# Performance work log

Hardware: AMD Instinct MI355X
Metric: run time of the kernel (lower is better)

## Reference

```python
import jax, jax.numpy as jnp
import numpy as np

NUM_NODES = 1_000_000
IN_FEATS = 128
NUM_GRAPHS = 1024
N_ITERS = 3


def setup_inputs() -> dict:
    key = jax.random.key(0)
    k1, k2, k3, k4, k5, k6 = jax.random.split(key, 6)
    H = IN_FEATS
    s = 1.0 / np.sqrt(H)
    x = jax.random.normal(k1, (NUM_NODES, H), dtype=jnp.float32)
    batch = jnp.sort(jax.random.randint(k2, (NUM_NODES,), 0, NUM_GRAPHS, dtype=jnp.int32))
    W_ih = jax.random.uniform(k3, (4 * H, 2 * H), minval=-s, maxval=s, dtype=jnp.float32)
    W_hh = jax.random.uniform(k4, (4 * H, H), minval=-s, maxval=s, dtype=jnp.float32)
    b_ih = jax.random.uniform(k5, (4 * H,), minval=-s, maxval=s, dtype=jnp.float32)
    b_hh = jax.random.uniform(k6, (4 * H,), minval=-s, maxval=s, dtype=jnp.float32)
    return {"x": x, "batch": batch, "W_ih": W_ih, "W_hh": W_hh, "b_ih": b_ih, "b_hh": b_hh}


def _lstm_cell(inp, h, c, W_ih, W_hh, b_ih, b_hh):
    # PyTorch gate order: i, f, g, o
    gates = inp @ W_ih.T + h @ W_hh.T + b_ih + b_hh  # (B, 4H)
    i, f, g, o = jnp.split(gates, 4, axis=-1)
    c_new = jax.nn.sigmoid(f) * c + jax.nn.sigmoid(i) * jnp.tanh(g)
    h_new = jax.nn.sigmoid(o) * jnp.tanh(c_new)
    return h_new, c_new


def reference(x, batch, W_ih, W_hh, b_ih, b_hh):
    H = IN_FEATS
    B = NUM_GRAPHS
    h = jnp.zeros((B, H), dtype=x.dtype)
    c = jnp.zeros((B, H), dtype=x.dtype)
    q_star = jnp.zeros((B, H), dtype=x.dtype)
    for _ in range(N_ITERS):  # small fixed iteration count
        q_exp = q_star[batch]                       # gather: (N, H)
        lstm_inp = jnp.concatenate([x, q_exp], -1)  # (N, 2H)
        pooled = jax.ops.segment_sum(lstm_inp, batch, num_segments=B)  # (B, 2H)
        h, c = _lstm_cell(pooled, h, c, W_ih, W_hh, b_ih, b_hh)
        q_star = h
    return jnp.concatenate([q_star, h], axis=-1)  # (B, 2H)
```

## Files before the change

### kernel.cpp

```cpp
#include <hip/hip_runtime.h>
#include <hip/hip_bf16.h>
#include <math.h>

#define H 128
#define NG 1024

__global__ void k0_bounds(const int* __restrict__ batch, int N, int* __restrict__ seg) {
    int i = blockIdx.x * blockDim.x + threadIdx.x;
    if (i >= N) return;
    int cur = batch[i];
    int prev = (i == 0) ? -1 : batch[i - 1];
    for (int b = prev + 1; b <= cur; ++b) seg[b] = i;
    if (i == N - 1) {
        for (int b = cur + 1; b <= NG; ++b) seg[b] = N;
    }
}

__global__ __launch_bounds__(128) void k1_seqsum(const float* __restrict__ x,
                                                 const int* __restrict__ seg,
                                                 float* __restrict__ sumx) {
    const int b = blockIdx.x;
    const int k = threadIdx.x;
    const int start = seg[b], end = seg[b + 1];

    const float* p = x + (size_t)start * H + k;
    float acc = 0.0f;
    int r = start;
    for (; r + 8 <= end; r += 8) {
        const float v0 = p[0 * H];
        const float v1 = p[1 * H];
        const float v2 = p[2 * H];
        const float v3 = p[3 * H];
        const float v4 = p[4 * H];
        const float v5 = p[5 * H];
        const float v6 = p[6 * H];
        const float v7 = p[7 * H];
        p += 8 * H;
        acc += v0; acc += v1; acc += v2; acc += v3;
        acc += v4; acc += v5; acc += v6; acc += v7;
    }
    for (; r < end; ++r) {
        acc += *p;
        p += H;
    }
    sumx[(size_t)b * H + k] = acc;
}

__device__ __forceinline__ double sigd(double v) { return 1.0 / (1.0 + exp(-v)); }

__global__ __launch_bounds__(512) void k2_lstm_pg(const float* __restrict__ sumx,
                                                  const int* __restrict__ seg,
                                                  const float* __restrict__ W_ih,
                                                  const float* __restrict__ W_hh,
                                                  const float* __restrict__ b_ih,
                                                  const float* __restrict__ b_hh,
                                                  float* __restrict__ out) {
    __shared__ float s_sx[H];
    __shared__ float s_pq[H];
    __shared__ float s_h[H];
    __shared__ float s_c[H];
    __shared__ float s_g[4 * H];

    const int b = blockIdx.x;
    const int r = threadIdx.x;
    const int cnt = seg[b + 1] - seg[b];

    if (r < H) {
        s_sx[r] = sumx[(size_t)b * H + r];
        s_pq[r] = 0.0f;
        s_h[r] = 0.0f;
        s_c[r] = 0.0f;
    }
    __syncthreads();

    const double bias = (double)b_ih[r] + (double)b_hh[r];
    const float* w1 = W_ih + (size_t)r * (2 * H);
    const float* wq = W_ih + (size_t)r * (2 * H) + H;
    const float* wh = W_hh + (size_t)r * H;

    for (int it = 0; it < 3; ++it) {
        double acc = bias;
        for (int k = 0; k < H; ++k) acc += (double)w1[k] * (double)s_sx[k];
        for (int k = 0; k < H; ++k) acc += (double)wq[k] * (double)s_pq[k];
        for (int k = 0; k < H; ++k) acc += (double)wh[k] * (double)s_h[k];
        s_g[r] = (float)acc;
        __syncthreads();

        if (r < H) {
            const double ig = (double)s_g[r];
            const double fg = (double)s_g[H + r];
            const double gg = (double)s_g[2 * H + r];
            const double og = (double)s_g[3 * H + r];
            const float c32 = (float)(sigd(fg) * (double)s_c[r] + sigd(ig) * tanh(gg));
            const float h32 = (float)(sigd(og) * tanh((double)c32));
            s_c[r] = c32;
            s_h[r] = h32;
        }
        __syncthreads();

        if (it < 2) {
            if (r < H) {
                const float qv = s_h[r];
                float s = 0.0f;
                for (int j = 0; j < cnt; ++j) s += qv;
                s_pq[r] = s;
            }
            __syncthreads();
        }
    }

    if (r < H) {
        const float hv = s_h[r];
        out[(size_t)b * (2 * H) + r] = hv;
        out[(size_t)b * (2 * H) + H + r] = hv;
    }
}

extern "C" void kernel_launch(void* const* d_in, const int* in_sizes, int n_in,
                              void* d_out, int out_size, void* d_ws, size_t ws_size,
                              hipStream_t stream) {
    const float* x     = (const float*)d_in[0];
    const int*   batch = (const int*)d_in[1];
    const float* W_ih  = (const float*)d_in[2];
    const float* W_hh  = (const float*)d_in[3];
    const float* b_ih  = (const float*)d_in[4];
    const float* b_hh  = (const float*)d_in[5];
    if (in_sizes[2] == 4 * H * H && in_sizes[3] == 8 * H * H) {
        const float* t = W_ih; W_ih = W_hh; W_hh = t;
    }
    float* out = (float*)d_out;

    const int N = in_sizes[1];

    int*   seg  = (int*)d_ws;
    float* sumx = (float*)((char*)d_ws + 8192);

    k0_bounds<<<(N + 255) / 256, 256, 0, stream>>>(batch, N, seg);
    k1_seqsum<<<NG, 128, 0, stream>>>(x, seg, sumx);
    k2_lstm_pg<<<NG, 512, 0, stream>>>(sumx, seg, W_ih, W_hh, b_ih, b_hh, out);
}
```

Measured before the change: 960.7 us.

## Batch four graphs per LSTM block with transposed weights and skip zero-state matvecs

Adds a transpose kernel so the LSTM weight reads are coalesced across threads (column-major by gate row). The LSTM kernel now processes four graphs per block, reusing each loaded weight across four accumulators, and skips the q/h matvecs on the first iteration, where those states are zero. It also fuses the q-sum step into the cell update to drop one barrier, and widens the seqsum unroll from 8 to 16 loads. In exchange it adds an extra kernel launch and workspace traffic for the transposed weights, plus more shared memory per block held in double precision.

```diff
diff --git a/kernel.cpp b/kernel.cpp
--- a/kernel.cpp
+++ b/kernel.cpp
@@ -4,6 +4,7 @@
 
 #define H 128
 #define NG 1024
+#define GPB 4
 
 __global__ void k0_bounds(const int* __restrict__ batch, int N, int* __restrict__ seg) {
     int i = blockIdx.x * blockDim.x + threadIdx.x;
@@ -16,6 +17,19 @@
     }
 }
 
+__global__ __launch_bounds__(256) void kT_transpose(const float* __restrict__ W_ih,
+                                                    const float* __restrict__ W_hh,
+                                                    float* __restrict__ WT1,
+                                                    float* __restrict__ WTq,
+                                                    float* __restrict__ WTh) {
+    const int idx = blockIdx.x * 256 + threadIdx.x;
+    const int k = idx >> 9;
+    const int r = idx & 511;
+    WT1[idx] = W_ih[(size_t)r * 256 + k];
+    WTq[idx] = W_ih[(size_t)r * 256 + 128 + k];
+    WTh[idx] = W_hh[(size_t)r * 128 + k];
+}
+
 __global__ __launch_bounds__(128) void k1_seqsum(const float* __restrict__ x,
                                                  const int* __restrict__ seg,
                                                  float* __restrict__ sumx) {
@@ -26,18 +40,13 @@
     const float* p = x + (size_t)start * H + k;
     float acc = 0.0f;
     int r = start;
-    for (; r + 8 <= end; r += 8) {
-        const float v0 = p[0 * H];
-        const float v1 = p[1 * H];
-        const float v2 = p[2 * H];
-        const float v3 = p[3 * H];
-        const float v4 = p[4 * H];
-        const float v5 = p[5 * H];
-        const float v6 = p[6 * H];
-        const float v7 = p[7 * H];
-        p += 8 * H;
-        acc += v0; acc += v1; acc += v2; acc += v3;
-        acc += v4; acc += v5; acc += v6; acc += v7;
+    for (; r + 16 <= end; r += 16) {
+        float v[16];
+#pragma unroll
+        for (int j = 0; j < 16; ++j) v[j] = p[j * H];
+        p += 16 * H;
+#pragma unroll
+        for (int j = 0; j < 16; ++j) acc += v[j];
     }
     for (; r < end; ++r) {
         acc += *p;
@@ -48,71 +57,92 @@
 
 __device__ __forceinline__ double sigd(double v) { return 1.0 / (1.0 + exp(-v)); }
 
-__global__ __launch_bounds__(512) void k2_lstm_pg(const float* __restrict__ sumx,
-                                                  const int* __restrict__ seg,
-                                                  const float* __restrict__ W_ih,
-                                                  const float* __restrict__ W_hh,
-                                                  const float* __restrict__ b_ih,
-                                                  const float* __restrict__ b_hh,
-                                                  float* __restrict__ out) {
-    __shared__ float s_sx[H];
-    __shared__ float s_pq[H];
-    __shared__ float s_h[H];
-    __shared__ float s_c[H];
-    __shared__ float s_g[4 * H];
+__global__ __launch_bounds__(512) void k2_lstm(const float* __restrict__ sumx,
+                                               const int* __restrict__ seg,
+                                               const float* __restrict__ WT1,
+                                               const float* __restrict__ WTq,
+                                               const float* __restrict__ WTh,
+                                               const float* __restrict__ b_ih,
+                                               const float* __restrict__ b_hh,
+                                               float* __restrict__ out) {
+    __shared__ double s_sx[GPB][H];
+    __shared__ double s_pq[GPB][H];
+    __shared__ double s_h64[GPB][H];
+    __shared__ float  s_h[GPB][H];
+    __shared__ float  s_c[GPB][H];
+    __shared__ float  s_g[GPB][4 * H];
+    __shared__ int    s_cnt[GPB];
 
-    const int b = blockIdx.x;
     const int r = threadIdx.x;
-    const int cnt = seg[b + 1] - seg[b];
+    const int g0 = blockIdx.x * GPB;
 
-    if (r < H) {
-        s_sx[r] = sumx[(size_t)b * H + r];
-        s_pq[r] = 0.0f;
-        s_h[r] = 0.0f;
-        s_c[r] = 0.0f;
+    if (r < GPB) s_cnt[r] = seg[g0 + r + 1] - seg[g0 + r];
+    {
+        const int g = r >> 7, f = r & 127;
+        const float v = sumx[(size_t)(g0 + g) * H + f];
+        s_sx[g][f] = (double)v;
+        s_pq[g][f] = 0.0;
+        s_h64[g][f] = 0.0;
+        s_h[g][f] = 0.0f;
+        s_c[g][f] = 0.0f;
     }
     __syncthreads();
 
     const double bias = (double)b_ih[r] + (double)b_hh[r];
-    const float* w1 = W_ih + (size_t)r * (2 * H);
-    const float* wq = W_ih + (size_t)r * (2 * H) + H;
-    const float* wh = W_hh + (size_t)r * H;
 
     for (int it = 0; it < 3; ++it) {
-        double acc = bias;
-        for (int k = 0; k < H; ++k) acc += (double)w1[k] * (double)s_sx[k];
-        for (int k = 0; k < H; ++k) acc += (double)wq[k] * (double)s_pq[k];
-        for (int k = 0; k < H; ++k) acc += (double)wh[k] * (double)s_h[k];
-        s_g[r] = (float)acc;
+        double acc[GPB];
+#pragma unroll
+        for (int g = 0; g < GPB; ++g) acc[g] = bias;
+
+        for (int k = 0; k < H; ++k) {
+            const double w = (double)WT1[k * 512 + r];
+#pragma unroll
+            for (int g = 0; g < GPB; ++g) acc[g] += w * s_sx[g][k];
+        }
+        if (it > 0) {
+            for (int k = 0; k < H; ++k) {
+                const double w = (double)WTq[k * 512 + r];
+#pragma unroll
+                for (int g = 0; g < GPB; ++g) acc[g] += w * s_pq[g][k];
+            }
+            for (int k = 0; k < H; ++k) {
+                const double w = (double)WTh[k * 512 + r];
+#pragma unroll
+                for (int g = 0; g < GPB; ++g) acc[g] += w * s_h64[g][k];
+            }
+        }
+#pragma unroll
+        for (int g = 0; g < GPB; ++g) s_g[g][r] = (float)acc[g];
         __syncthreads();
 
-        if (r < H) {
-            const double ig = (double)s_g[r];
-            const double fg = (double)s_g[H + r];
-            const double gg = (double)s_g[2 * H + r];
-            const double og = (double)s_g[3 * H + r];
-            const float c32 = (float)(sigd(fg) * (double)s_c[r] + sigd(ig) * tanh(gg));
+        {
+            const int g = r >> 7, f = r & 127;
+            const double ig = (double)s_g[g][f];
+            const double fg = (double)s_g[g][H + f];
+            const double gg = (double)s_g[g][2 * H + f];
+            const double og = (double)s_g[g][3 * H + f];
+            const float c32 = (float)(sigd(fg) * (double)s_c[g][f] + sigd(ig) * tanh(gg));
             const float h32 = (float)(sigd(og) * tanh((double)c32));
-            s_c[r] = c32;
-            s_h[r] = h32;
+            s_c[g][f] = c32;
+            s_h[g][f] = h32;
+            s_h64[g][f] = (double)h32;
+            if (it < 2) {
+                const float qv = h32;
+                const int cnt = s_cnt[g];
+                float s = 0.0f;
+                for (int j = 0; j < cnt; ++j) s += qv;
+                s_pq[g][f] = (double)s;
+            }
         }
         __syncthreads();
-
-        if (it < 2) {
-            if (r < H) {
-                const float qv = s_h[r];
-                float s = 0.0f;
-                for (int j = 0; j < cnt; ++j) s += qv;
-                s_pq[r] = s;
-            }
-            __syncthreads();
-        }
     }
 
-    if (r < H) {
-        const float hv = s_h[r];
-        out[(size_t)b * (2 * H) + r] = hv;
-        out[(size_t)b * (2 * H) + H + r] = hv;
+    {
+        const int g = r >> 7, f = r & 127;
+        const float hv = s_h[g][f];
+        out[(size_t)(g0 + g) * (2 * H) + f] = hv;
+        out[(size_t)(g0 + g) * (2 * H) + H + f] = hv;
     }
 }
 
@@ -134,8 +164,12 @@
 
     int*   seg  = (int*)d_ws;
     float* sumx = (float*)((char*)d_ws + 8192);
+    float* WT1  = (float*)((char*)d_ws + 540672);
+    float* WTq  = (float*)((char*)d_ws + 802816);
+    float* WTh  = (float*)((char*)d_ws + 1064960);
 
+    kT_transpose<<<256, 256, 0, stream>>>(W_ih, W_hh, WT1, WTq, WTh);
     k0_bounds<<<(N + 255) / 256, 256, 0, stream>>>(batch, N, seg);
     k1_seqsum<<<NG, 128, 0, stream>>>(x, seg, sumx);
-    k2_lstm_pg<<<NG, 512, 0, stream>>>(sumx, seg, W_ih, W_hh, b_ih, b_hh, out);
+    k2_lstm<<<NG / GPB, 512, 0, stream>>>(sumx, seg, WT1, WTq, WTh, b_ih, b_hh, out);
 }
```

Result: faster. 774.8 us (-19.4%).
